# Performance work log

Hardware: AMD Instinct MI355X
Metric: run time of the kernel (lower is better)

## Reference

```python
import jax, jax.numpy as jnp
import numpy as np

N = 50000        # nodes
E = 800000       # edges (before self loops)
F_IN = 78        # num_features_xd
H1 = 10          # heads of gcn1
OUT2 = 128       # output_dim of gcn2
G = 512          # graphs in batch
NEG_SLOPE = 0.2  # PyG GATConv default


def setup_inputs() -> dict:
    key = jax.random.key(0)
    ks = jax.random.split(key, 16)
    def glorot(k, shape, fan_in):
        return jax.random.normal(k, shape, jnp.float32) * (1.0 / np.sqrt(fan_in))
    inp = {}
    inp['x'] = jax.random.normal(ks[0], (N, F_IN), jnp.float32)
    inp['edge_index'] = jax.random.randint(ks[1], (2, E), 0, N, dtype=jnp.int32)
    inp['batch'] = jnp.sort(jax.random.randint(ks[2], (N,), 0, G, dtype=jnp.int32))
    inp['num_graphs'] = G
    # gcn1: GATConv(78 -> 78, heads=10, concat=True)
    inp['W1'] = glorot(ks[3], (F_IN, H1 * F_IN), F_IN)
    inp['a_src1'] = glorot(ks[4], (H1, F_IN), F_IN)
    inp['a_dst1'] = glorot(ks[5], (H1, F_IN), F_IN)
    inp['b1'] = jnp.zeros((H1 * F_IN,), jnp.float32)
    # gcn2: GATConv(780 -> 128, heads=1)
    inp['W2'] = glorot(ks[6], (H1 * F_IN, OUT2), H1 * F_IN)
    inp['a_src2'] = glorot(ks[7], (1, OUT2), OUT2)
    inp['a_dst2'] = glorot(ks[8], (1, OUT2), OUT2)
    inp['b2'] = jnp.zeros((OUT2,), jnp.float32)
    # fc_g1: Linear(128 -> 128)
    inp['fcW'] = glorot(ks[9], (OUT2, OUT2), OUT2)
    inp['fcb'] = jnp.zeros((OUT2,), jnp.float32)
    return inp


def _gat_layer(x, src, dst, W, a_src, a_dst, b, heads, out_dim):
    # x: [N, Fin] -> h: [N, heads, out_dim]
    n = x.shape[0]
    h = (x @ W).reshape(n, heads, out_dim)
    # per-node attention projections: [N, heads]
    alpha_src = jnp.einsum('nhf,hf->nh', h, a_src)
    alpha_dst = jnp.einsum('nhf,hf->nh', h, a_dst)
    # per-edge logits (message from src j to dst i): [Etot, heads]
    e = jax.nn.leaky_relu(alpha_src[src] + alpha_dst[dst], NEG_SLOPE)
    # segment softmax over edges grouped by destination node
    m = jax.ops.segment_max(e, dst, num_segments=n)
    m = jnp.where(jnp.isfinite(m), m, 0.0)
    ex = jnp.exp(e - m[dst])
    denom = jax.ops.segment_sum(ex, dst, num_segments=n)
    alpha = ex / (denom[dst] + 1e-16)
    # weighted message scatter: [N, heads, out_dim]
    out = jax.ops.segment_sum(h[src] * alpha[:, :, None], dst, num_segments=n)
    return out.reshape(n, heads * out_dim) + b


def reference(x, edge_index, batch, num_graphs, W1, a_src1, a_dst1, b1,
              W2, a_src2, a_dst2, b2, fcW, fcb):
    n = x.shape[0]
    # PyG GATConv add_self_loops=True
    loops = jnp.arange(n, dtype=edge_index.dtype)
    src = jnp.concatenate([edge_index[0], loops])
    dst = jnp.concatenate([edge_index[1], loops])
    # eval mode: dropouts are identity
    h = jax.nn.relu(_gat_layer(x, src, dst, W1, a_src1, a_dst1, b1, H1, F_IN))
    h = jax.nn.relu(_gat_layer(h, src, dst, W2, a_src2, a_dst2, b2, 1, OUT2))
    # global max pool over graphs
    pooled = jax.ops.segment_max(h, batch, num_segments=num_graphs)
    pooled = jnp.where(jnp.isfinite(pooled), pooled, 0.0)
    return jax.nn.relu(pooled @ fcW + fcb)
```

## Files before the change

### kernel.cpp

```cpp
#include <hip/hip_runtime.h>
#include <hip/hip_bf16.h>
#include <stdint.h>

typedef unsigned int uint32;
typedef unsigned short u16;
typedef __attribute__((ext_vector_type(8))) short bf16x8;
typedef __attribute__((ext_vector_type(4))) float f32x4;
typedef __attribute__((ext_vector_type(2))) float f32x2;
typedef uint32 u32x4 __attribute__((ext_vector_type(4)));

#define N_NODES 50000
#define NP      50048
#define N_EDGES 800000
#define ETOT    (N_EDGES + N_NODES)
#define F_INN   78
#define H1      10
#define D1      780
#define OUT2    128
#define NGRAPH  512
#define NEG_SLOPE 0.2f
#define PL40    ((size_t)NP * 40)

__device__ __forceinline__ float lrelu(float v) { return v > 0.f ? v : NEG_SLOPE * v; }
__device__ __forceinline__ u16 f2bfbits(float f) {
    return __bfloat16_as_ushort(__float2bfloat16(f));
}
__device__ __forceinline__ uint32 packbf(float lo, float hi) {
    return (uint32)f2bfbits(lo) | ((uint32)f2bfbits(hi) << 16);
}
__device__ __forceinline__ f32x2 bf2(uint32 u) {
    __hip_bfloat162 b = *reinterpret_cast<__hip_bfloat162*>(&u);
    float2 t = __bfloat1622float2(b);
    return (f32x2){t.x, t.y};
}
__device__ __forceinline__ int esrc(const int* ei, int e) { return e < N_EDGES ? ei[e] : e - N_EDGES; }
__device__ __forceinline__ int edst(const int* ei, int e) { return e < N_EDGES ? ei[N_EDGES + e] : e - N_EDGES; }

typedef __attribute__((address_space(1))) const uint32 guint;
typedef __attribute__((address_space(3))) uint32 luint;
__device__ __forceinline__ void cp16(uint32* lds, const uint32* g, int lane) {
    __builtin_amdgcn_global_load_lds((guint*)(g + lane * 4), (luint*)lds, 16, 0, 0);
}

#define NXP (N_NODES * 80)
__global__ __launch_bounds__(256) void prep_kernel(const float* __restrict__ x,
                                                   const float* __restrict__ W1,
                                                   const float* __restrict__ W2,
                                                   u16* __restrict__ xbp,
                                                   u16* __restrict__ w1p,
                                                   u16* __restrict__ w2p) {
    const int total = NXP + 10 * 80 * 80 + 10 * 128 * 80;
    for (int id = blockIdx.x * 256 + threadIdx.x; id < total; id += gridDim.x * 256) {
        if (id < NXP) {
            int n = id / 80, k = id - n * 80;
            xbp[id] = (k < 78) ? f2bfbits(x[n * 78 + k]) : ((k == 78) ? (u16)0x3F80 : (u16)0);
        } else if (id < NXP + 64000) {
            int t = id - NXP;
            int h = t / 6400, r = t - h * 6400;
            int n = r / 80, k = r - n * 80;
            w1p[t] = (n < 78 && k < 78) ? f2bfbits(W1[k * D1 + h * 78 + n]) : (u16)0;
        } else {
            int t = id - NXP - 64000;
            int h = t / 10240, r = t - h * 10240;
            int n = r / 80, k = r - n * 80;
            w2p[t] = (k < 78) ? f2bfbits(W2[(h * 78 + k) * OUT2 + n]) : (u16)0;
        }
    }
}

__global__ __launch_bounds__(256) void prep2_kernel(const float* __restrict__ W1,
                                                    const float* __restrict__ a_src1,
                                                    const float* __restrict__ a_dst1,
                                                    const float* __restrict__ W2,
                                                    const float* __restrict__ a_src2,
                                                    const float* __restrict__ a_dst2,
                                                    u16* __restrict__ VAT,
                                                    float* __restrict__ w2as,
                                                    float* __restrict__ w2ad) {
    int gid = blockIdx.x * 256 + threadIdx.x;
    int gs = gridDim.x * 256;
    for (int idx = gid; idx < 32 * 80; idx += gs) {
        int j = idx / 80, k = idx - j * 80;
        float s = 0.f;
        if (j < 20 && k < 78) {
            int h = (j < 10) ? j : j - 10;
            const float* vec = ((j < 10) ? a_src1 : a_dst1) + h * F_INN;
            const float* wrow = W1 + k * D1 + h * F_INN;
            for (int f = 0; f < F_INN; ++f) s = fmaf(wrow[f], vec[f], s);
            VAT[idx] = f2bfbits(s);
        } else {
            VAT[idx] = 0;
        }
    }
    for (int c = gid; c < D1; c += gs) {
        const float* r0 = W2 + (size_t)c * OUT2;
        float s = 0.f, d = 0.f;
        for (int j = 0; j < OUT2; ++j) {
            s = fmaf(r0[j], a_src2[j], s);
            d = fmaf(r0[j], a_dst2[j], d);
        }
        w2as[c] = s;
        w2ad[c] = d;
    }
}

__global__ __launch_bounds__(256) void alphas1x_kernel(const uint32* __restrict__ xbu,
                                                       const uint32* __restrict__ vatu,
                                                       float* __restrict__ asd1,
                                                       float* __restrict__ asrc) {
    __shared__ uint32 As[5136];
    __shared__ uint32 Bs[1296];
    int tid = threadIdx.x, lane = tid & 63, wv = tid >> 6;
    int row0 = blockIdx.x * 128;
    const uint32* aplane = xbu + (size_t)row0 * 40;

#pragma unroll
    for (int t = 0; t < 5; ++t)
        cp16(As + wv * 1280 + t * 256, aplane + wv * 1280 + t * 256, lane);
    if (wv == 0) {
#pragma unroll
        for (int t = 0; t < 5; ++t)
            cp16(Bs + t * 256, vatu + t * 256, lane);
    }
    __syncthreads();

    int l15 = lane & 15, quad = lane >> 4;
    const u16* Asu = (const u16*)As;
    const u16* Bsu = (const u16*)Bs;
    f32x4 acc[2][2];
#pragma unroll
    for (int mi = 0; mi < 2; ++mi)
#pragma unroll
        for (int nj = 0; nj < 2; ++nj) acc[mi][nj] = (f32x4){0.f, 0.f, 0.f, 0.f};

    int abase[2], bbase[2];
#pragma unroll
    for (int mi = 0; mi < 2; ++mi) abase[mi] = (wv * 32 + mi * 16 + l15) * 80 + quad * 8;
#pragma unroll
    for (int nj = 0; nj < 2; ++nj) bbase[nj] = (nj * 16 + l15) * 80 + quad * 8;

    bf16x8 z8 = {0, 0, 0, 0, 0, 0, 0, 0};
#pragma unroll
    for (int ks = 0; ks < 96; ks += 32) {
        bf16x8 a[2], b[2];
#pragma unroll
        for (int mi = 0; mi < 2; ++mi) {
            a[mi] = *(const bf16x8*)(Asu + abase[mi] + ks);
            if (ks == 64 && quad >= 2) a[mi] = z8;
        }
#pragma unroll
        for (int nj = 0; nj < 2; ++nj) b[nj] = *(const bf16x8*)(Bsu + bbase[nj] + ks);
#pragma unroll
        for (int mi = 0; mi < 2; ++mi)
#pragma unroll
            for (int nj = 0; nj < 2; ++nj)
                acc[mi][nj] = __builtin_amdgcn_mfma_f32_16x16x32_bf16(a[mi], b[nj], acc[mi][nj], 0, 0, 0);
    }

#pragma unroll
    for (int mi = 0; mi < 2; ++mi)
#pragma unroll
        for (int nj = 0; nj < 2; ++nj) {
            int col = nj * 16 + l15;
            if (col < 20) {
#pragma unroll
                for (int reg = 0; reg < 4; ++reg) {
                    int row = row0 + wv * 32 + mi * 16 + quad * 4 + reg;
                    if (row < N_NODES) {
                        asd1[(size_t)row * 20 + col] = acc[mi][nj][reg];
                        if (col < 10) asrc[(size_t)row * 12 + col] = acc[mi][nj][reg];
                    }
                }
            }
        }
}

__global__ void hist_kernel(const int* __restrict__ ei, int* __restrict__ deg) {
    int e = blockIdx.x * 256 + threadIdx.x;
    if (e < ETOT) atomicAdd(&deg[edst(ei, e)], 1);
}

__global__ __launch_bounds__(256) void scan1_kernel(const int* __restrict__ deg,
                                                    int* __restrict__ row_ptr,
                                                    int* __restrict__ bsum) {
    __shared__ int buf[256];
    int tid = threadIdx.x;
    int i = blockIdx.x * 256 + tid;
    int v = (i < N_NODES) ? deg[i] : 0;
    buf[tid] = v;
    __syncthreads();
    for (int off = 1; off < 256; off <<= 1) {
        int t = (tid >= off) ? buf[tid - off] : 0;
        __syncthreads();
        buf[tid] += t;
        __syncthreads();
    }
    if (i < N_NODES) row_ptr[i] = buf[tid] - v;
    if (tid == 255) bsum[blockIdx.x] = buf[255];
}

__global__ __launch_bounds__(256) void scan2_kernel(const int* __restrict__ bsum,
                                                    int* __restrict__ boff) {
    __shared__ int buf[256];
    int tid = threadIdx.x;
    int v = (tid < 196) ? bsum[tid] : 0;
    buf[tid] = v;
    __syncthreads();
    for (int off = 1; off < 256; off <<= 1) {
        int t = (tid >= off) ? buf[tid - off] : 0;
        __syncthreads();
        buf[tid] += t;
        __syncthreads();
    }
    if (tid < 196) boff[tid] = buf[tid] - v;
}

__global__ __launch_bounds__(256) void scan3_kernel(int* __restrict__ row_ptr,
                                                    const int* __restrict__ boff,
                                                    int* __restrict__ cursor) {
    int i = blockIdx.x * 256 + threadIdx.x;
    if (i < N_NODES) {
        int r = row_ptr[i] + boff[blockIdx.x];
        row_ptr[i] = r;
        cursor[i] = r;
    }
    if (i == 0) row_ptr[N_NODES] = ETOT;
}

__global__ void scatter_kernel(const int* __restrict__ ei, int* __restrict__ cursor,
                               u16* __restrict__ src_arr) {
    int e = blockIdx.x * 256 + threadIdx.x;
    if (e < ETOT) {
        int d = edst(ei, e);
        int pos = atomicAdd(&cursor[d], 1);
        src_arr[pos] = (u16)esrc(ei, e);
    }
}

__global__ __launch_bounds__(256) void agg1m_kernel(const int* __restrict__ row_ptr,
                                                    const u16* __restrict__ src_arr,
                                                    const float* __restrict__ asrc,
                                                    const float* __restrict__ asd1,
                                                    const uint32* __restrict__ xbu,
                                                    u16* __restrict__ aggb16) {
    __shared__ uint32 S[4][1960];
    int tid = threadIdx.x, lane = tid & 63, wv = tid >> 6;
    int i = blockIdx.x * 4 + wv;
    int rs = row_ptr[i], deg = row_ptr[i + 1] - rs;
    uint32* xt32 = S[wv];
    uint32* wm32 = xt32 + 1600;
    int* sv = (int*)(xt32 + 1920);
    int l15 = lane & 15, quad = lane >> 4;
    int slot = lane & 31, half = lane >> 5;
    u32x4 z4 = {0, 0, 0, 0};
    if (lane < 30) *(u32x4*)(wm32 + 200 + lane * 4) = z4;
    uint32 selv = (l15 & 1) ? 0x07060302u : 0x05040100u;

    float dstv[10];
#pragma unroll
    for (int q = 0; q < 10; ++q) dstv[q] = asd1[(size_t)i * 20 + 10 + q];

    int hp = l15 >> 1;
    int pa1 = (quad * 8 + 4 * hp) & 31;
    int pa2 = (pa1 + 4) & 31;

    f32x4 acc[5];
#pragma unroll
    for (int nt = 0; nt < 5; ++nt) acc[nt] = (f32x4){0.f, 0.f, 0.f, 0.f};

    for (int base = 0; base < deg; base += 32) {
        int cnt = min(deg - base, 32);
        if (lane < cnt) sv[lane] = (int)src_arr[rs + base + lane];
        __builtin_amdgcn_wave_barrier();
        int srow = (slot < cnt) ? sv[slot] : 0;
        const float* arow = asrc + (size_t)srow * 12;
        if (half == 0) {
            float4 a01 = *(const float4*)(arow);
            float2 a2  = *(const float2*)(arow + 4);
            uint32 u0 = 0, u1 = 0, u2 = 0;
            if (slot < cnt) {
                u0 = packbf(__expf(lrelu(a01.x + dstv[0])), __expf(lrelu(a01.y + dstv[1])));
                u1 = packbf(__expf(lrelu(a01.z + dstv[2])), __expf(lrelu(a01.w + dstv[3])));
                u2 = packbf(__expf(lrelu(a2.x + dstv[4])),  __expf(lrelu(a2.y + dstv[5])));
            }
            wm32[0 * 40 + (slot & 31)] = u0;
            wm32[1 * 40 + ((slot + 4) & 31)] = u1;
            wm32[2 * 40 + ((slot + 8) & 31)] = u2;
        } else {
            float2 a3 = *(const float2*)(arow + 6);
            float2 a4 = *(const float2*)(arow + 8);
            uint32 u3 = 0, u4 = 0;
            if (slot < cnt) {
                u3 = packbf(__expf(lrelu(a3.x + dstv[6])), __expf(lrelu(a3.y + dstv[7])));
                u4 = packbf(__expf(lrelu(a4.x + dstv[8])), __expf(lrelu(a4.y + dstv[9])));
            }
            wm32[3 * 40 + ((slot + 12) & 31)] = u3;
            wm32[4 * 40 + ((slot + 16) & 31)] = u4;
        }
#pragma unroll
        for (int t = 0; t < 5; ++t) {
            int c4 = 2 * t + half;
            u32x4 v = z4;
            if (slot < cnt) v = *(const u32x4*)(xbu + (size_t)srow * 40 + c4 * 4);
            uint32* rowp = xt32 + (4 * c4) * 40;
#pragma unroll
            for (int k = 0; k < 4; ++k)
                rowp[k * 40 + ((slot + 16 * c4 + 4 * k) & 31)] = v[k];
        }
        __builtin_amdgcn_wave_barrier();
        int arow2 = hp * 40;
        u32x4 a0 = *(const u32x4*)(wm32 + arow2 + pa1);
        u32x4 a1 = *(const u32x4*)(wm32 + arow2 + pa2);
        u32x4 au = {__builtin_amdgcn_perm(a0[1], a0[0], selv),
                    __builtin_amdgcn_perm(a0[3], a0[2], selv),
                    __builtin_amdgcn_perm(a1[1], a1[0], selv),
                    __builtin_amdgcn_perm(a1[3], a1[2], selv)};
        bf16x8 af = *(bf16x8*)&au;
#pragma unroll
        for (int nt = 0; nt < 5; ++nt) {
            int browb = (nt * 8 + hp) * 40;
            u32x4 b0 = *(const u32x4*)(xt32 + browb + pa1);
            u32x4 b1 = *(const u32x4*)(xt32 + browb + pa2);
            u32x4 bu = {__builtin_amdgcn_perm(b0[1], b0[0], selv),
                        __builtin_amdgcn_perm(b0[3], b0[2], selv),
                        __builtin_amdgcn_perm(b1[1], b1[0], selv),
                        __builtin_amdgcn_perm(b1[3], b1[2], selv)};
            bf16x8 bf = *(bf16x8*)&bu;
            acc[nt] = __builtin_amdgcn_mfma_f32_16x16x32_bf16(af, bf, acc[nt], 0, 0, 0);
        }
        __builtin_amdgcn_wave_barrier();
    }

    float rden[4];
#pragma unroll
    for (int reg = 0; reg < 4; ++reg) {
        float d = __shfl(acc[4][reg], (lane & 48) | 14, 64);
        rden[reg] = __builtin_amdgcn_rcpf(d);
    }
    size_t nb = (size_t)i * 80 + l15;
#pragma unroll
    for (int reg = 0; reg < 4; ++reg) {
        int head = quad * 4 + reg;
        if (head < 10) {
            u16* hpn = aggb16 + (size_t)head * (size_t)PL40 * 2 + nb;
#pragma unroll
            for (int nt = 0; nt < 5; ++nt) {
                float v = acc[nt][reg] * rden[reg];
                u16 b = f2bfbits(v);
                if (nt == 4 && l15 >= 14) b = 0;
                hpn[nt * 16] = b;
            }
        }
    }
}

__global__ __launch_bounds__(256) void gemm1b_kernel(const uint32* __restrict__ aggb,
                                                     const uint32* __restrict__ w1p,
                                                     const float* __restrict__ b1,
                                                     const float* __restrict__ w2as,
                                                     const float* __restrict__ w2ad,
                                                     uint32* __restrict__ out1p,
                                                     float* __restrict__ asp,
                                                     float* __restrict__ adp) {
    __shared__ uint32 As[5136];
    __shared__ uint32 Bs[3336];
    int tid = threadIdx.x, lane = tid & 63, wv = tid >> 6;
    int row0 = blockIdx.x * 128;
    int h = blockIdx.y;
    const uint32* aplane = aggb + (size_t)h * PL40 + (size_t)row0 * 40;
    const uint32* wplane = w1p + (size_t)h * 3200;

#pragma unroll
    for (int t = 0; t < 5; ++t)
        cp16(As + wv * 1280 + t * 256, aplane + wv * 1280 + t * 256, lane);
    int tw0 = wv * 3, tw1 = (wv == 3) ? 13 : wv * 3 + 3;
    for (int t = tw0; t < tw1; ++t)
        cp16(Bs + t * 256, wplane + t * 256, lane);
    __syncthreads();

    int l15 = lane & 15, quad = lane >> 4;
    const u16* Asu = (const u16*)As;
    const u16* Bsu = (const u16*)Bs;

    f32x4 acc[2][5];
#pragma unroll
    for (int mi = 0; mi < 2; ++mi)
#pragma unroll
        for (int nj = 0; nj < 5; ++nj) acc[mi][nj] = (f32x4){0.f, 0.f, 0.f, 0.f};

    int abase[2], bbase[5];
#pragma unroll
    for (int mi = 0; mi < 2; ++mi) abase[mi] = (wv * 32 + mi * 16 + l15) * 80 + quad * 8;
#pragma unroll
    for (int nj = 0; nj < 5; ++nj) bbase[nj] = (nj * 16 + l15) * 80 + quad * 8;

    bf16x8 z8 = {0, 0, 0, 0, 0, 0, 0, 0};
#pragma unroll
    for (int ks = 0; ks < 96; ks += 32) {
        bf16x8 a[2], b[5];
#pragma unroll
        for (int mi = 0; mi < 2; ++mi) {
            a[mi] = *(const bf16x8*)(Asu + abase[mi] + ks);
            if (ks == 64 && quad >= 2) a[mi] = z8;
        }
#pragma unroll
        for (int nj = 0; nj < 5; ++nj) b[nj] = *(const bf16x8*)(Bsu + bbase[nj] + ks);
#pragma unroll
        for (int mi = 0; mi < 2; ++mi)
#pragma unroll
            for (int nj = 0; nj < 5; ++nj)
                acc[mi][nj] = __builtin_amdgcn_mfma_f32_16x16x32_bf16(a[mi], b[nj], acc[mi][nj], 0, 0, 0);
    }

    __syncthreads();
    u16* Cw = (u16*)As;
    float s2p[2][4] = {}, d2p[2][4] = {};
#pragma unroll
    for (int mi = 0; mi < 2; ++mi) {
        int rl0 = wv * 32 + mi * 16 + quad * 4;
#pragma unroll
        for (int nj = 0; nj < 5; ++nj) {
            int col = nj * 16 + l15;
            if (col < 78) {
                int gc = h * 78 + col;
                float bia = b1[gc], was = w2as[gc], wad = w2ad[gc];
#pragma unroll
                for (int reg = 0; reg < 4; ++reg) {
                    float v = fmaxf(acc[mi][nj][reg] + bia, 0.f);
                    Cw[(rl0 + reg) * 80 + col] = f2bfbits(v);
                    s2p[mi][reg] = fmaf(v, was, s2p[mi][reg]);
                    d2p[mi][reg] = fmaf(v, wad, d2p[mi][reg]);
                }
            } else {
#pragma unroll
                for (int reg = 0; reg < 4; ++reg) Cw[(rl0 + reg) * 80 + col] = 0;
            }
        }
    }
#pragma unroll
    for (int off = 1; off < 16; off <<= 1)
#pragma unroll
        for (int mi = 0; mi < 2; ++mi)
#pragma unroll
            for (int reg = 0; reg < 4; ++reg) {
                s2p[mi][reg] += __shfl_xor(s2p[mi][reg], off, 64);
                d2p[mi][reg] += __shfl_xor(d2p[mi][reg], off, 64);
            }
    if (l15 == 0) {
#pragma unroll
        for (int mi = 0; mi < 2; ++mi) {
            int rowb = row0 + wv * 32 + mi * 16 + quad * 4;
#pragma unroll
            for (int reg = 0; reg < 4; ++reg) {
                int r = rowb + reg;
                if (r < N_NODES) {
                    asp[(size_t)h * N_NODES + r] = s2p[mi][reg];
                    adp[(size_t)h * N_NODES + r] = d2p[mi][reg];
                }
            }
        }
    }
    __syncthreads();
    uint32* oplane = out1p + (size_t)h * PL40 + (size_t)row0 * 40;
#pragma unroll
    for (int jj = 0; jj < 5; ++jj) {
        int idx = jj * 256 + tid;
        *(u32x4*)(oplane + 4 * idx) = *(const u32x4*)(As + 4 * idx);
    }
}

__global__ __launch_bounds__(256) void sum10_kernel(const float* __restrict__ asp,
                                                    const float* __restrict__ adp,
                                                    float* __restrict__ as2,
                                                    float* __restrict__ ad2) {
    int n = blockIdx.x * 256 + threadIdx.x;
    if (n >= N_NODES) return;
    float s = 0.f, d = 0.f;
#pragma unroll
    for (int h = 0; h < 10; ++h) {
        s += asp[(size_t)h * N_NODES + n];
        d += adp[(size_t)h * N_NODES + n];
    }
    as2[n] = s;
    ad2[n] = d;
}

__global__ __launch_bounds__(256) void gemm2_mfma(const uint32* __restrict__ out1p,
                                                  const uint32* __restrict__ w2p,
                                                  u16* __restrict__ h2) {
    __shared__ uint32 As[2576];
    __shared__ uint32 Bs[5136];
    int tid = threadIdx.x, lane = tid & 63, wv = tid >> 6;
    int row0 = blockIdx.x * 64;
    int l15 = lane & 15, quad = lane >> 4;
    const u16* Asu = (const u16*)As;
    const u16* Bsu = (const u16*)Bs;

    f32x4 acc[8];
#pragma unroll
    for (int nj = 0; nj < 8; ++nj) acc[nj] = (f32x4){0.f, 0.f, 0.f, 0.f};

    int abase = (wv * 16 + l15) * 80 + quad * 8;
    int bbase[8];
#pragma unroll
    for (int nj = 0; nj < 8; ++nj) bbase[nj] = (nj * 16 + l15) * 80 + quad * 8;
    bf16x8 z8 = {0, 0, 0, 0, 0, 0, 0, 0};

    for (int h = 0; h < 10; ++h) {
        const uint32* aplane = out1p + (size_t)h * PL40 + (size_t)row0 * 40;
        const uint32* bplane = w2p + (size_t)h * 5120;
        for (int t = wv; t < 10; t += 4)
            cp16(As + t * 256, aplane + t * 256, lane);
#pragma unroll
        for (int t = 0; t < 5; ++t)
            cp16(Bs + (wv * 5 + t) * 256, bplane + (wv * 5 + t) * 256, lane);
        __syncthreads();
#pragma unroll
        for (int ks = 0; ks < 96; ks += 32) {
            bf16x8 a = *(const bf16x8*)(Asu + abase + ks);
            if (ks == 64 && quad >= 2) a = z8;
#pragma unroll
            for (int nj = 0; nj < 8; ++nj) {
                bf16x8 b = *(const bf16x8*)(Bsu + bbase[nj] + ks);
                acc[nj] = __builtin_amdgcn_mfma_f32_16x16x32_bf16(a, b, acc[nj], 0, 0, 0);
            }
        }
        __syncthreads();
    }

#pragma unroll
    for (int nj = 0; nj < 8; ++nj) {
        int col = nj * 16 + l15;
#pragma unroll
        for (int reg = 0; reg < 4; ++reg) {
            int r = row0 + wv * 16 + quad * 4 + reg;
            if (r < N_NODES) h2[(size_t)r * OUT2 + col] = f2bfbits(acc[nj][reg]);
        }
    }
}

__global__ __launch_bounds__(256) void agg2_kernel(const int* __restrict__ row_ptr,
                                                   const u16* __restrict__ src_arr,
                                                   const float* __restrict__ as2,
                                                   const float* __restrict__ ad2,
                                                   const uint32* __restrict__ h2u,
                                                   const float* __restrict__ b2,
                                                   const int* __restrict__ batch,
                                                   float* __restrict__ pooled) {
    __shared__ float w_sh[4][64];
    __shared__ int src_sh[4][64];
    __shared__ float red[4][128];
    __shared__ int gsh[4];
    int tid = threadIdx.x, lane = tid & 63, wv = tid >> 6;
    int i = blockIdx.x * 4 + wv;
    int rs = row_ptr[i], deg = row_ptr[i + 1] - rs;
    float ad2i = ad2[i];

    f32x2 acc = {0.f, 0.f};
    float den = 0.f;
    if (deg <= 64) {
        if (lane < deg) {
            int s = (int)src_arr[rs + lane];
            float w = __expf(lrelu(as2[s] + ad2i));
            den = w;
            w_sh[wv][lane] = w;
            src_sh[wv][lane] = s;
        }
        __builtin_amdgcn_wave_barrier();
#pragma unroll
        for (int off = 1; off < 64; off <<= 1) den += __shfl_xor(den, off, 64);
        float rden = __builtin_amdgcn_rcpf(den);
        int cnt = deg, eix = 0;
        for (; eix + 3 < cnt; eix += 4) {
            int s0 = src_sh[wv][eix], s1 = src_sh[wv][eix + 1];
            int s2 = src_sh[wv][eix + 2], s3 = src_sh[wv][eix + 3];
            float w0 = w_sh[wv][eix], w1 = w_sh[wv][eix + 1];
            float w2v = w_sh[wv][eix + 2], w3 = w_sh[wv][eix + 3];
            uint32 u0 = h2u[(size_t)s0 * 64 + lane];
            uint32 u1 = h2u[(size_t)s1 * 64 + lane];
            uint32 u2 = h2u[(size_t)s2 * 64 + lane];
            uint32 u3 = h2u[(size_t)s3 * 64 + lane];
            acc = w0 * bf2(u0) + acc;
            acc = w1 * bf2(u1) + acc;
            acc = w2v * bf2(u2) + acc;
            acc = w3 * bf2(u3) + acc;
        }
        for (; eix < cnt; ++eix) {
            int s0 = src_sh[wv][eix];
            float w0 = w_sh[wv][eix];
            uint32 u0 = h2u[(size_t)s0 * 64 + lane];
            acc = w0 * bf2(u0) + acc;
        }
        acc *= rden;
    } else {
        for (int eix = lane; eix < deg; eix += 64)
            den += __expf(lrelu(as2[(int)src_arr[rs + eix]] + ad2i));
#pragma unroll
        for (int off = 1; off < 64; off <<= 1) den += __shfl_xor(den, off, 64);
        float rden = __builtin_amdgcn_rcpf(den);
        for (int base = 0; base < deg; base += 64) {
            int cnt = min(deg - base, 64);
            if (lane < cnt) {
                int s = (int)src_arr[rs + base + lane];
                w_sh[wv][lane] = __expf(lrelu(as2[s] + ad2i));
                src_sh[wv][lane] = s;
            }
            __builtin_amdgcn_wave_barrier();
            int eix = 0;
            for (; eix + 3 < cnt; eix += 4) {
                int s0 = src_sh[wv][eix], s1 = src_sh[wv][eix + 1];
                int s2 = src_sh[wv][eix + 2], s3 = src_sh[wv][eix + 3];
                float w0 = w_sh[wv][eix], w1 = w_sh[wv][eix + 1];
                float w2v = w_sh[wv][eix + 2], w3 = w_sh[wv][eix + 3];
                uint32 u0 = h2u[(size_t)s0 * 64 + lane];
                uint32 u1 = h2u[(size_t)s1 * 64 + lane];
                uint32 u2 = h2u[(size_t)s2 * 64 + lane];
                uint32 u3 = h2u[(size_t)s3 * 64 + lane];
                acc = w0 * bf2(u0) + acc;
                acc = w1 * bf2(u1) + acc;
                acc = w2v * bf2(u2) + acc;
                acc = w3 * bf2(u3) + acc;
            }
            for (; eix < cnt; ++eix) {
                int s0 = src_sh[wv][eix];
                float w0 = w_sh[wv][eix];
                uint32 u0 = h2u[(size_t)s0 * 64 + lane];
                acc = w0 * bf2(u0) + acc;
            }
            __builtin_amdgcn_wave_barrier();
        }
        acc *= rden;
    }
    float2 bv = ((const float2*)b2)[lane];
    float v0 = fmaxf(acc.x + bv.x, 0.f);
    float v1 = fmaxf(acc.y + bv.y, 0.f);
    int g = batch[i];
    red[wv][2 * lane] = v0;
    red[wv][2 * lane + 1] = v1;
    if (lane == 0) gsh[wv] = g;
    __syncthreads();
    bool leader = true;
#pragma unroll
    for (int w2i = 0; w2i < 3; ++w2i)
        if (w2i < wv && gsh[w2i] == g) leader = false;
    if (leader) {
        float m0 = v0, m1 = v1;
#pragma unroll
        for (int w2i = 1; w2i < 4; ++w2i) {
            if (w2i > wv && gsh[w2i] == g) {
                m0 = fmaxf(m0, red[w2i][2 * lane]);
                m1 = fmaxf(m1, red[w2i][2 * lane + 1]);
            }
        }
        atomicMax((int*)&pooled[g * OUT2 + 2 * lane], __float_as_int(m0));
        atomicMax((int*)&pooled[g * OUT2 + 2 * lane + 1], __float_as_int(m1));
    }
}

__global__ __launch_bounds__(128) void fc_kernel(const float* __restrict__ pooled,
                                                 const float* __restrict__ fcW,
                                                 const float* __restrict__ fcb,
                                                 float* __restrict__ out) {
    int g = blockIdx.x, tid = threadIdx.x;
    __shared__ float p[128];
    p[tid] = pooled[g * OUT2 + tid];
    __syncthreads();
    float acc = fcb[tid];
    for (int k = 0; k < 128; ++k) acc = fmaf(p[k], fcW[k * OUT2 + tid], acc);
    out[g * OUT2 + tid] = fmaxf(acc, 0.f);
}

extern "C" void kernel_launch(void* const* d_in, const int* in_sizes, int n_in,
                              void* d_out, int out_size, void* d_ws, size_t ws_size,
                              hipStream_t stream) {
    const float* x      = (const float*)d_in[0];
    const int*   ei     = (const int*)d_in[1];
    const int*   batch  = (const int*)d_in[2];
    const float* W1     = (const float*)d_in[4];
    const float* a_src1 = (const float*)d_in[5];
    const float* a_dst1 = (const float*)d_in[6];
    const float* b1     = (const float*)d_in[7];
    const float* W2     = (const float*)d_in[8];
    const float* a_src2 = (const float*)d_in[9];
    const float* a_dst2 = (const float*)d_in[10];
    const float* b2     = (const float*)d_in[11];
    const float* fcW    = (const float*)d_in[12];
    const float* fcb    = (const float*)d_in[13];
    float* out = (float*)d_out;

    size_t off = 0;
    char* base = (char*)d_ws;
    auto alloc = [&](size_t bytes) -> void* {
        void* p = base + off;
        off += (bytes + 255) & ~(size_t)255;
        return p;
    };
    uint32* aggb  = (uint32*)alloc(PL40 * 10 * 4);
    uint32* out1p = (uint32*)alloc(PL40 * 10 * 4);
    u16* h2arena  = (u16*)alloc((size_t)N_NODES * OUT2 * 2);
    u16* h2   = h2arena;
    u16* xbp  = h2arena;
    float* asd1 = (float*)alloc((size_t)N_NODES * 20 * 4);
    float* asp  = asd1;
    float* adp  = asd1 + (size_t)10 * N_NODES;
    float* asrc = (float*)alloc((size_t)N_NODES * 12 * 4);
    float* as2  = (float*)alloc((size_t)N_NODES * 4);
    float* ad2  = (float*)alloc((size_t)N_NODES * 4);
    u16* w1p    = (u16*)alloc((size_t)(10 * 80 * 80) * 2 + 1024);
    u16* w2p    = (u16*)alloc((size_t)(10 * 128 * 80) * 2);
    u16* VAT    = (u16*)alloc((size_t)32 * 80 * 2);
    float* w2as = (float*)alloc((size_t)D1 * 4);
    float* w2ad = (float*)alloc((size_t)D1 * 4);
    float* pooled = (float*)alloc((size_t)NGRAPH * OUT2 * 4);
    int* deg     = (int*)alloc((size_t)N_NODES * 4);
    int* row_ptr = (int*)alloc((size_t)(N_NODES + 1) * 4);
    int* cursor  = (int*)alloc((size_t)N_NODES * 4);
    u16* src_arr = (u16*)alloc((size_t)ETOT * 2);
    int* bsum    = (int*)alloc(196 * 4);
    int* boff    = (int*)alloc(196 * 4);

    hipMemsetAsync(deg, 0, (size_t)N_NODES * 4, stream);
    hipMemsetAsync(pooled, 0, (size_t)NGRAPH * OUT2 * 4, stream);

    prep_kernel<<<2048, 256, 0, stream>>>(x, W1, W2, xbp, w1p, w2p);
    prep2_kernel<<<8, 256, 0, stream>>>(W1, a_src1, a_dst1, W2, a_src2, a_dst2,
                                        VAT, w2as, w2ad);
    alphas1x_kernel<<<391, 256, 0, stream>>>((const uint32*)xbp, (const uint32*)VAT,
                                             asd1, asrc);
    hist_kernel<<<(ETOT + 255) / 256, 256, 0, stream>>>(ei, deg);
    scan1_kernel<<<196, 256, 0, stream>>>(deg, row_ptr, bsum);
    scan2_kernel<<<1, 256, 0, stream>>>(bsum, boff);
    scan3_kernel<<<196, 256, 0, stream>>>(row_ptr, boff, cursor);
    scatter_kernel<<<(ETOT + 255) / 256, 256, 0, stream>>>(ei, cursor, src_arr);
    agg1m_kernel<<<N_NODES / 4, 256, 0, stream>>>(row_ptr, src_arr, asrc, asd1,
                                                  (const uint32*)xbp, (u16*)aggb);
    gemm1b_kernel<<<dim3(391, 10), 256, 0, stream>>>(aggb, (const uint32*)w1p,
                                                     b1, w2as, w2ad,
                                                     out1p, asp, adp);
    sum10_kernel<<<196, 256, 0, stream>>>(asp, adp, as2, ad2);
    gemm2_mfma<<<782, 256, 0, stream>>>(out1p, (const uint32*)w2p, h2);
    agg2_kernel<<<N_NODES / 4, 256, 0, stream>>>(row_ptr, src_arr, as2, ad2,
                                                 (const uint32*)h2, b2, batch, pooled);
    fc_kernel<<<NGRAPH, 128, 0, stream>>>(pooled, fcW, fcb, out);
}
```

Measured before the change: 353.8 us.

## Fuse layer-1 GEMM, alpha reduction and layer-2 GEMM into one kernel

Merges gemm1b, sum10 and gemm2 into a single kernel that loops over the 10 heads per 64-row tile. Each head's post-ReLU layer-1 output is kept in shared memory and fed straight into the layer-2 MFMA, and the attention projections are accumulated across heads in registers. This removes the global round trip of the 780-wide intermediate (out1p) and the per-head asp/adp partials, plus two launches. In exchange, each block serially reloads W1 and W2 planes per head, uses more LDS per block (fewer resident blocks), and runs only 782 blocks.

```diff
diff --git a/kernel.cpp b/kernel.cpp
--- a/kernel.cpp
+++ b/kernel.cpp
@@ -354,70 +354,70 @@
     }
 }
 
-__global__ __launch_bounds__(256) void gemm1b_kernel(const uint32* __restrict__ aggb,
-                                                     const uint32* __restrict__ w1p,
-                                                     const float* __restrict__ b1,
-                                                     const float* __restrict__ w2as,
-                                                     const float* __restrict__ w2ad,
-                                                     uint32* __restrict__ out1p,
-                                                     float* __restrict__ asp,
-                                                     float* __restrict__ adp) {
-    __shared__ uint32 As[5136];
-    __shared__ uint32 Bs[3336];
+__global__ __launch_bounds__(256) void gemmf_kernel(const uint32* __restrict__ aggb,
+                                                    const uint32* __restrict__ w1p,
+                                                    const uint32* __restrict__ w2p,
+                                                    const float* __restrict__ b1,
+                                                    const float* __restrict__ w2as,
+                                                    const float* __restrict__ w2ad,
+                                                    u16* __restrict__ h2,
+                                                    float* __restrict__ as2,
+                                                    float* __restrict__ ad2) {
+    __shared__ uint32 As[2576];
+    __shared__ uint32 Bs1[3336];
+    __shared__ uint32 Bs2[5136];
+    __shared__ uint32 C1s[2576];
     int tid = threadIdx.x, lane = tid & 63, wv = tid >> 6;
-    int row0 = blockIdx.x * 128;
-    int h = blockIdx.y;
-    const uint32* aplane = aggb + (size_t)h * PL40 + (size_t)row0 * 40;
-    const uint32* wplane = w1p + (size_t)h * 3200;
-
-#pragma unroll
-    for (int t = 0; t < 5; ++t)
-        cp16(As + wv * 1280 + t * 256, aplane + wv * 1280 + t * 256, lane);
-    int tw0 = wv * 3, tw1 = (wv == 3) ? 13 : wv * 3 + 3;
-    for (int t = tw0; t < tw1; ++t)
-        cp16(Bs + t * 256, wplane + t * 256, lane);
-    __syncthreads();
-
+    int row0 = blockIdx.x * 64;
     int l15 = lane & 15, quad = lane >> 4;
     const u16* Asu = (const u16*)As;
-    const u16* Bsu = (const u16*)Bs;
-
-    f32x4 acc[2][5];
-#pragma unroll
-    for (int mi = 0; mi < 2; ++mi)
-#pragma unroll
-        for (int nj = 0; nj < 5; ++nj) acc[mi][nj] = (f32x4){0.f, 0.f, 0.f, 0.f};
-
-    int abase[2], bbase[5];
-#pragma unroll
-    for (int mi = 0; mi < 2; ++mi) abase[mi] = (wv * 32 + mi * 16 + l15) * 80 + quad * 8;
-#pragma unroll
-    for (int nj = 0; nj < 5; ++nj) bbase[nj] = (nj * 16 + l15) * 80 + quad * 8;
-
+    const u16* B1u = (const u16*)Bs1;
+    const u16* B2u = (const u16*)Bs2;
+    const u16* C1u = (const u16*)C1s;
+    u16* Cw = (u16*)C1s;
+
+    f32x4 acc2[8];
+#pragma unroll
+    for (int nj = 0; nj < 8; ++nj) acc2[nj] = (f32x4){0.f, 0.f, 0.f, 0.f};
+    float s2p[4] = {}, d2p[4] = {};
+
+    int abase = (wv * 16 + l15) * 80 + quad * 8;
+    int b1base[5];
+#pragma unroll
+    for (int nj = 0; nj < 5; ++nj) b1base[nj] = (nj * 16 + l15) * 80 + quad * 8;
+    int b2base[8];
+#pragma unroll
+    for (int nj = 0; nj < 8; ++nj) b2base[nj] = (nj * 16 + l15) * 80 + quad * 8;
     bf16x8 z8 = {0, 0, 0, 0, 0, 0, 0, 0};
-#pragma unroll
-    for (int ks = 0; ks < 96; ks += 32) {
-        bf16x8 a[2], b[5];
-#pragma unroll
-        for (int mi = 0; mi < 2; ++mi) {
-            a[mi] = *(const bf16x8*)(Asu + abase[mi] + ks);
-            if (ks == 64 && quad >= 2) a[mi] = z8;
-        }
-#pragma unroll
-        for (int nj = 0; nj < 5; ++nj) b[nj] = *(const bf16x8*)(Bsu + bbase[nj] + ks);
-#pragma unroll
-        for (int mi = 0; mi < 2; ++mi)
-#pragma unroll
-            for (int nj = 0; nj < 5; ++nj)
-                acc[mi][nj] = __builtin_amdgcn_mfma_f32_16x16x32_bf16(a[mi], b[nj], acc[mi][nj], 0, 0, 0);
-    }
-
-    __syncthreads();
-    u16* Cw = (u16*)As;
-    float s2p[2][4] = {}, d2p[2][4] = {};
-#pragma unroll
-    for (int mi = 0; mi < 2; ++mi) {
-        int rl0 = wv * 32 + mi * 16 + quad * 4;
+    int rl0 = wv * 16 + quad * 4;
+
+    for (int h = 0; h < 10; ++h) {
+        const uint32* aplane = aggb + (size_t)h * PL40 + (size_t)row0 * 40;
+        const uint32* w1pl = w1p + (size_t)h * 3200;
+        const uint32* w2pl = w2p + (size_t)h * 5120;
+        for (int t = wv; t < 10; t += 4)
+            cp16(As + t * 256, aplane + t * 256, lane);
+        int tw0 = wv * 3, tw1 = (wv == 3) ? 13 : wv * 3 + 3;
+        for (int t = tw0; t < tw1; ++t)
+            cp16(Bs1 + t * 256, w1pl + t * 256, lane);
+#pragma unroll
+        for (int t = 0; t < 5; ++t)
+            cp16(Bs2 + (wv * 5 + t) * 256, w2pl + (wv * 5 + t) * 256, lane);
+        __syncthreads();
+
+        f32x4 acc1[5];
+#pragma unroll
+        for (int nj = 0; nj < 5; ++nj) acc1[nj] = (f32x4){0.f, 0.f, 0.f, 0.f};
+#pragma unroll
+        for (int ks = 0; ks < 96; ks += 32) {
+            bf16x8 a = *(const bf16x8*)(Asu + abase + ks);
+            if (ks == 64 && quad >= 2) a = z8;
+#pragma unroll
+            for (int nj = 0; nj < 5; ++nj) {
+                bf16x8 b = *(const bf16x8*)(B1u + b1base[nj] + ks);
+                acc1[nj] = __builtin_amdgcn_mfma_f32_16x16x32_bf16(a, b, acc1[nj], 0, 0, 0);
+            }
+        }
 #pragma unroll
         for (int nj = 0; nj < 5; ++nj) {
             int col = nj * 16 + l15;
@@ -426,103 +426,25 @@
                 float bia = b1[gc], was = w2as[gc], wad = w2ad[gc];
 #pragma unroll
                 for (int reg = 0; reg < 4; ++reg) {
-                    float v = fmaxf(acc[mi][nj][reg] + bia, 0.f);
+                    float v = fmaxf(acc1[nj][reg] + bia, 0.f);
                     Cw[(rl0 + reg) * 80 + col] = f2bfbits(v);
-                    s2p[mi][reg] = fmaf(v, was, s2p[mi][reg]);
-                    d2p[mi][reg] = fmaf(v, wad, d2p[mi][reg]);
+                    s2p[reg] = fmaf(v, was, s2p[reg]);
+                    d2p[reg] = fmaf(v, wad, d2p[reg]);
                 }
             } else {
 #pragma unroll
                 for (int reg = 0; reg < 4; ++reg) Cw[(rl0 + reg) * 80 + col] = 0;
             }
         }
-    }
-#pragma unroll
-    for (int off = 1; off < 16; off <<= 1)
-#pragma unroll
-        for (int mi = 0; mi < 2; ++mi)
-#pragma unroll
-            for (int reg = 0; reg < 4; ++reg) {
-                s2p[mi][reg] += __shfl_xor(s2p[mi][reg], off, 64);
-                d2p[mi][reg] += __shfl_xor(d2p[mi][reg], off, 64);
-            }
-    if (l15 == 0) {
-#pragma unroll
-        for (int mi = 0; mi < 2; ++mi) {
-            int rowb = row0 + wv * 32 + mi * 16 + quad * 4;
-#pragma unroll
-            for (int reg = 0; reg < 4; ++reg) {
-                int r = rowb + reg;
-                if (r < N_NODES) {
-                    asp[(size_t)h * N_NODES + r] = s2p[mi][reg];
-                    adp[(size_t)h * N_NODES + r] = d2p[mi][reg];
-                }
-            }
-        }
-    }
-    __syncthreads();
-    uint32* oplane = out1p + (size_t)h * PL40 + (size_t)row0 * 40;
-#pragma unroll
-    for (int jj = 0; jj < 5; ++jj) {
-        int idx = jj * 256 + tid;
-        *(u32x4*)(oplane + 4 * idx) = *(const u32x4*)(As + 4 * idx);
-    }
-}
-
-__global__ __launch_bounds__(256) void sum10_kernel(const float* __restrict__ asp,
-                                                    const float* __restrict__ adp,
-                                                    float* __restrict__ as2,
-                                                    float* __restrict__ ad2) {
-    int n = blockIdx.x * 256 + threadIdx.x;
-    if (n >= N_NODES) return;
-    float s = 0.f, d = 0.f;
-#pragma unroll
-    for (int h = 0; h < 10; ++h) {
-        s += asp[(size_t)h * N_NODES + n];
-        d += adp[(size_t)h * N_NODES + n];
-    }
-    as2[n] = s;
-    ad2[n] = d;
-}
-
-__global__ __launch_bounds__(256) void gemm2_mfma(const uint32* __restrict__ out1p,
-                                                  const uint32* __restrict__ w2p,
-                                                  u16* __restrict__ h2) {
-    __shared__ uint32 As[2576];
-    __shared__ uint32 Bs[5136];
-    int tid = threadIdx.x, lane = tid & 63, wv = tid >> 6;
-    int row0 = blockIdx.x * 64;
-    int l15 = lane & 15, quad = lane >> 4;
-    const u16* Asu = (const u16*)As;
-    const u16* Bsu = (const u16*)Bs;
-
-    f32x4 acc[8];
-#pragma unroll
-    for (int nj = 0; nj < 8; ++nj) acc[nj] = (f32x4){0.f, 0.f, 0.f, 0.f};
-
-    int abase = (wv * 16 + l15) * 80 + quad * 8;
-    int bbase[8];
-#pragma unroll
-    for (int nj = 0; nj < 8; ++nj) bbase[nj] = (nj * 16 + l15) * 80 + quad * 8;
-    bf16x8 z8 = {0, 0, 0, 0, 0, 0, 0, 0};
-
-    for (int h = 0; h < 10; ++h) {
-        const uint32* aplane = out1p + (size_t)h * PL40 + (size_t)row0 * 40;
-        const uint32* bplane = w2p + (size_t)h * 5120;
-        for (int t = wv; t < 10; t += 4)
-            cp16(As + t * 256, aplane + t * 256, lane);
-#pragma unroll
-        for (int t = 0; t < 5; ++t)
-            cp16(Bs + (wv * 5 + t) * 256, bplane + (wv * 5 + t) * 256, lane);
-        __syncthreads();
+        __builtin_amdgcn_wave_barrier();
 #pragma unroll
         for (int ks = 0; ks < 96; ks += 32) {
-            bf16x8 a = *(const bf16x8*)(Asu + abase + ks);
+            bf16x8 a = *(const bf16x8*)(C1u + abase + ks);
             if (ks == 64 && quad >= 2) a = z8;
 #pragma unroll
             for (int nj = 0; nj < 8; ++nj) {
-                bf16x8 b = *(const bf16x8*)(Bsu + bbase[nj] + ks);
-                acc[nj] = __builtin_amdgcn_mfma_f32_16x16x32_bf16(a, b, acc[nj], 0, 0, 0);
+                bf16x8 b = *(const bf16x8*)(B2u + b2base[nj] + ks);
+                acc2[nj] = __builtin_amdgcn_mfma_f32_16x16x32_bf16(a, b, acc2[nj], 0, 0, 0);
             }
         }
         __syncthreads();
@@ -533,8 +455,25 @@
         int col = nj * 16 + l15;
 #pragma unroll
         for (int reg = 0; reg < 4; ++reg) {
-            int r = row0 + wv * 16 + quad * 4 + reg;
-            if (r < N_NODES) h2[(size_t)r * OUT2 + col] = f2bfbits(acc[nj][reg]);
+            int r = row0 + rl0 + reg;
+            if (r < N_NODES) h2[(size_t)r * OUT2 + col] = f2bfbits(acc2[nj][reg]);
+        }
+    }
+#pragma unroll
+    for (int off = 1; off < 16; off <<= 1)
+#pragma unroll
+        for (int reg = 0; reg < 4; ++reg) {
+            s2p[reg] += __shfl_xor(s2p[reg], off, 64);
+            d2p[reg] += __shfl_xor(d2p[reg], off, 64);
+        }
+    if (l15 == 0) {
+#pragma unroll
+        for (int reg = 0; reg < 4; ++reg) {
+            int r = row0 + rl0 + reg;
+            if (r < N_NODES) {
+                as2[r] = s2p[reg];
+                ad2[r] = d2p[reg];
+            }
         }
     }
 }
@@ -696,13 +635,10 @@
         return p;
     };
     uint32* aggb  = (uint32*)alloc(PL40 * 10 * 4);
-    uint32* out1p = (uint32*)alloc(PL40 * 10 * 4);
     u16* h2arena  = (u16*)alloc((size_t)N_NODES * OUT2 * 2);
     u16* h2   = h2arena;
     u16* xbp  = h2arena;
     float* asd1 = (float*)alloc((size_t)N_NODES * 20 * 4);
-    float* asp  = asd1;
-    float* adp  = asd1 + (size_t)10 * N_NODES;
     float* asrc = (float*)alloc((size_t)N_NODES * 12 * 4);
     float* as2  = (float*)alloc((size_t)N_NODES * 4);
     float* ad2  = (float*)alloc((size_t)N_NODES * 4);
@@ -734,11 +670,8 @@
     scatter_kernel<<<(ETOT + 255) / 256, 256, 0, stream>>>(ei, cursor, src_arr);
     agg1m_kernel<<<N_NODES / 4, 256, 0, stream>>>(row_ptr, src_arr, asrc, asd1,
                                                   (const uint32*)xbp, (u16*)aggb);
-    gemm1b_kernel<<<dim3(391, 10), 256, 0, stream>>>(aggb, (const uint32*)w1p,
-                                                     b1, w2as, w2ad,
-                                                     out1p, asp, adp);
-    sum10_kernel<<<196, 256, 0, stream>>>(asp, adp, as2, ad2);
-    gemm2_mfma<<<782, 256, 0, stream>>>(out1p, (const uint32*)w2p, h2);
+    gemmf_kernel<<<NP / 64, 256, 0, stream>>>(aggb, (const uint32*)w1p, (const uint32*)w2p,
+                                              b1, w2as, w2ad, h2, as2, ad2);
     agg2_kernel<<<N_NODES / 4, 256, 0, stream>>>(row_ptr, src_arr, as2, ad2,
                                                  (const uint32*)h2, b2, batch, pooled);
     fc_kernel<<<NGRAPH, 128, 0, stream>>>(pooled, fcW, fcb, out);
```

New measurement: 345.4 us. -2.4%, faster.
